# Optimization experiments

Hardware: AMD Instinct MI355X
Metric: run time of the kernel (lower is better)

Reference implementation:

```python
import jax, jax.numpy as jnp
import numpy as np

N = 200_000      # active voxels
C_IN = 128
C_OUT = 128
GRID = 128
K = 27           # 3x3x3 submanifold kernel offsets
EPS = 1e-4       # scn BatchNormalization default eps
LEAK = 0.333     # scn LeakyReLU default leakiness


def _build_neighbor_idx(rng):
    # unique active voxel coords via unique linear keys in GRID^3
    keys = rng.choice(GRID ** 3, size=N, replace=False).astype(np.int64)
    z = keys % GRID
    y = (keys // GRID) % GRID
    x = keys // (GRID * GRID)
    coords = np.stack([x, y, z], axis=1)  # [N,3]
    order = np.argsort(keys)
    sorted_keys = keys[order]
    offs = np.array([(dx, dy, dz) for dx in (-1, 0, 1)
                     for dy in (-1, 0, 1) for dz in (-1, 0, 1)], dtype=np.int64)
    nb = np.full((N, K), -1, dtype=np.int32)
    for k in range(K):
        q = coords + offs[k]  # [N,3]
        inb = np.all((q >= 0) & (q < GRID), axis=1)
        qk = (q[:, 0] * GRID + q[:, 1]) * GRID + q[:, 2]
        pos = np.searchsorted(sorted_keys, qk)
        pos = np.clip(pos, 0, N - 1)
        hit = inb & (sorted_keys[pos] == qk)
        nb[:, k] = np.where(hit, order[pos].astype(np.int32), -1)
    return nb


def setup_inputs() -> dict:
    key = jax.random.key(0)
    k1, k2 = jax.random.split(key)
    rng = np.random.default_rng(0)
    neighbor_idx = jnp.asarray(_build_neighbor_idx(rng))       # [N,27] int32, -1 = inactive
    features = jax.random.normal(k1, (N, C_IN), dtype=jnp.float32)
    # per-offset conv weights, scn-style init scale
    W = jax.random.normal(k2, (K, C_IN, C_OUT), dtype=jnp.float32) * (1.0 / np.sqrt(K * C_IN))
    b = jnp.zeros((C_OUT,), dtype=jnp.float32)
    gamma = jnp.ones((C_OUT,), dtype=jnp.float32)
    beta = jnp.zeros((C_OUT,), dtype=jnp.float32)
    return {"features": features, "W": W, "b": b, "gamma": gamma,
            "beta": beta, "neighbor_idx": neighbor_idx}


def reference(features, W, b, gamma, beta, neighbor_idx):
    # Submanifold 3D conv: output only at active sites; gather active neighbors.
    valid = (neighbor_idx >= 0)                      # [N,27] bool
    idx = jnp.where(valid, neighbor_idx, 0)          # safe gather index
    out = jnp.broadcast_to(b, (features.shape[0], C_OUT))
    for k in range(K):  # fixed structural loop over 27 kernel offsets
        xk = features[idx[:, k]] * valid[:, k:k + 1].astype(features.dtype)  # [N,C_IN]
        out = out + xk @ W[k]                                                # [N,C_OUT]
    # BatchNormalization over all active sites (training-mode batch stats)
    mean = jnp.mean(out, axis=0)
    var = jnp.var(out, axis=0)
    out = (out - mean) * jax.lax.rsqrt(var + EPS) * gamma + beta
    # LeakyReLU (scn default leakiness 0.333)
    return jnp.where(out > 0, out, LEAK * out)
```

## Files before the change

kernel.cpp:

```cpp
#include <hip/hip_runtime.h>
#include <hip/hip_bf16.h>

#define N_VOX 200000
#define CI 128
#define CO 128
#define KK 27
#define BM 128
#define NBLK 1563
#define NSTEP 54
#define LEAK 0.333f
#define BN_EPS 1e-4f
#define SENT 0x3FFFFu
#define ACC_STRIDE 132

typedef unsigned short u16;
typedef unsigned int u32;
typedef __attribute__((ext_vector_type(8))) short short8;
typedef __attribute__((ext_vector_type(4))) float f32x4;

typedef const __attribute__((address_space(1))) u32* gptr_t;
typedef __attribute__((address_space(3))) u32* lptr_t;

__device__ __forceinline__ u16 f2bf(float f) {
  union { float f; u32 u; } x; x.f = f;
  return (u16)((x.u + 0x7FFFu + ((x.u >> 16) & 1u)) >> 16);
}
__device__ __forceinline__ u16 cvt_bf(float f) {
  union { __hip_bfloat16 h; u16 u; } c;
  c.h = __float2bfloat16(f);
  return c.u;
}

__global__ __launch_bounds__(256) void fcast_kernel(const float* __restrict__ f,
                                                    u16* __restrict__ fb) {
  size_t i = ((size_t)blockIdx.x * 256 + threadIdx.x) * 8;
  float4 a = *(const float4*)(f + i);
  float4 b = *(const float4*)(f + i + 4);
  u16 t[8];
  t[0] = cvt_bf(a.x); t[1] = cvt_bf(a.y); t[2] = cvt_bf(a.z); t[3] = cvt_bf(a.w);
  t[4] = cvt_bf(b.x); t[5] = cvt_bf(b.y); t[6] = cvt_bf(b.z); t[7] = cvt_bf(b.w);
  *(uint4*)(fb + i) = *(const uint4*)t;
}

__global__ __launch_bounds__(256) void wcast3_kernel(const float* __restrict__ W,
                                                     u16* __restrict__ Wt3) {
  int gid = blockIdx.x * 256 + threadIdx.x;
  int lane = gid & 63, chunk = gid >> 6;
  int ks = chunk & 3, nf = (chunk >> 2) & 7, k = chunk >> 5;
  int lr = lane & 15, lg = lane >> 4;
  int co = nf * 16 + lr;
  int ci0 = ks * 32 + lg * 8;
  const float* Wk = W + (size_t)k * CI * CO;
  u16 t[8];
#pragma unroll
  for (int e = 0; e < 8; ++e) t[e] = f2bf(Wk[(ci0 + e) * CO + co]);
  *(uint4*)(Wt3 + (size_t)gid * 8) = *(const uint4*)t;
}

__global__ __launch_bounds__(256, 2) void conv_sp_kernel(
    const u16* __restrict__ featb, const u16* __restrict__ Wt3,
    const int* __restrict__ nb, const u16* __restrict__ zp,
    float* __restrict__ out, float* __restrict__ partial) {
  __shared__ __align__(16) char smem[75776];
  float* const accf = (float*)smem;
  u32* const rb_lds = (u32*)(smem + 67584);
  int* const cnt_lds = (int*)(smem + 74752);
  int* const wcnt = (int*)(smem + 74864);
  u32* const wl = (u32*)(smem + 74880);
  int* const wl_n = (int*)(smem + 75360);
  float* const ps = (float*)(smem + 67584);

  const int tid = threadIdx.x;
  const int bid = blockIdx.x;
  const int row0 = bid * BM;
  const int lane = tid & 63;
  const int w = tid >> 6;

  {
    f32x4 z4 = {0.f, 0.f, 0.f, 0.f};
    for (int i = tid; i < (BM * ACC_STRIDE) / 4; i += 256) ((f32x4*)accf)[i] = z4;
  }

  {
    const bool inrow = (tid < 128) && (row0 + tid < N_VOX);
    const int* nbp = nb + (size_t)(row0 + tid) * KK;
    int vv[KK];
#pragma unroll
    for (int k = 0; k < KK; ++k) vv[k] = (k != 13 && inrow) ? nbp[k] : -1;
    if (tid < 128)
      rb_lds[832 + tid] = ((u32)tid << 18) | (inrow ? (u32)(row0 + tid) : SENT);
    if (tid == 0) cnt_lds[13] = 128;
#pragma unroll
    for (int k = 0; k < KK; ++k) {
      if (k == 13) continue;
      bool valid = vv[k] >= 0;
      unsigned long long m = __ballot(valid);
      if (lane == 0) wcnt[w] = (int)__popcll(m);
      __syncthreads();
      int pos = (int)__popcll(m & ((1ull << lane) - 1ull)) + (w == 1 ? wcnt[0] : 0);
      int cnt = wcnt[0] + wcnt[1]; if (cnt > 64) cnt = 64;
      int kbase = (k < 13) ? k * 64 : 960 + (k - 14) * 64;
      if (valid && pos < 64) rb_lds[kbase + pos] = ((u32)tid << 18) | (u32)vv[k];
      int pe = (cnt + 15) & ~15;
      for (int i = cnt + tid; i < pe; i += 256) rb_lds[kbase + i] = SENT;
      if (tid == 0) cnt_lds[k] = cnt;
      __syncthreads();
    }
  }

  if (tid == 0) {
    int n = 0;
    for (int k = 0; k < KK; ++k) {
      int cnt = cnt_lds[k];
      int kbase = (k < 13) ? k * 64 : (k == 13 ? 832 : 960 + (k - 14) * 64);
      int ntk = (cnt + 15) >> 4;
      for (int t = 0; t < ntk; ++t) wl[n++] = ((u32)k << 11) | (u32)(kbase + t * 16);
    }
    wl_n[0] = n;
  }
  __syncthreads();

  const int wv = w;
  const int lr = lane & 15, lg = lane >> 4;
  const int colbase = wv * 32 + lr;
  const int nt = wl_n[0];

  auto rbRead = [&](u32 d, u32& es, uint4& sc) {
    int off = (int)(d & 0x7FFu);
    es = rb_lds[off + lr];
    sc = *(const uint4*)&rb_lds[off + lg * 4];
  };
  auto issueA = [&](u32 es, short8* a) {
    u32 src = es & SENT;
    const u16* ap = (src == SENT) ? zp : (featb + (size_t)src * CI);
#pragma unroll
    for (int ks = 0; ks < 4; ++ks) a[ks] = *(const short8*)(ap + ks * 32 + lg * 8);
  };
  auto issueB = [&](u32 d, short8* b) {
    int k = (int)(d >> 11);
    const u16* wb = Wt3 + (size_t)(k * 32 + wv * 8) * 512 + lane * 8;
#pragma unroll
    for (int j = 0; j < 8; ++j) b[j] = *(const short8*)(wb + j * 512);
  };
  auto computeT = [&](const short8* a, const short8* b, f32x4& c0, f32x4& c1) {
#pragma unroll
    for (int ks = 0; ks < 4; ++ks) {
      c0 = __builtin_amdgcn_mfma_f32_16x16x32_bf16(a[ks], b[ks], c0, 0, 0, 0);
      c1 = __builtin_amdgcn_mfma_f32_16x16x32_bf16(a[ks], b[4 + ks], c1, 0, 0, 0);
    }
  };
  auto scat1 = [&](u32 e2, float v0, float v1) {
    if (e2 != SENT) {
      int dr = (int)(e2 >> 18);
      accf[dr * ACC_STRIDE + colbase] += v0;
      accf[dr * ACC_STRIDE + colbase + 16] += v1;
    }
  };

  {
    u32 es0, es1; uint4 sc0, sc1;
    short8 a0[4], a1[4], b0v[8], b1v[8];
    u32 d0 = wl[0], d1 = wl[1];
    rbRead(d0, es0, sc0);
    rbRead(d1, es1, sc1);
    issueA(es0, a0); issueB(d0, b0v);
    issueA(es1, a1); issueB(d1, b1v);
    int i = 0;
    for (; i + 1 < nt; i += 2) {
      {
        u32 dn = wl[(i + 2 < nt) ? i + 2 : 0];
        u32 esn; uint4 scn; rbRead(dn, esn, scn);
        f32x4 c0 = {0.f, 0.f, 0.f, 0.f}, c1 = {0.f, 0.f, 0.f, 0.f};
        computeT(a0, b0v, c0, c1);
        issueA(esn, a0); issueB(dn, b0v);
        scat1(sc0.x, c0[0], c1[0]); scat1(sc0.y, c0[1], c1[1]);
        scat1(sc0.z, c0[2], c1[2]); scat1(sc0.w, c0[3], c1[3]);
        sc0 = scn;
      }
      {
        u32 dn = wl[(i + 3 < nt) ? i + 3 : 0];
        u32 esn; uint4 scn; rbRead(dn, esn, scn);
        f32x4 c0 = {0.f, 0.f, 0.f, 0.f}, c1 = {0.f, 0.f, 0.f, 0.f};
        computeT(a1, b1v, c0, c1);
        issueA(esn, a1); issueB(dn, b1v);
        scat1(sc1.x, c0[0], c1[0]); scat1(sc1.y, c0[1], c1[1]);
        scat1(sc1.z, c0[2], c1[2]); scat1(sc1.w, c0[3], c1[3]);
        sc1 = scn;
      }
    }
    if (i < nt) {
      f32x4 c0 = {0.f, 0.f, 0.f, 0.f}, c1 = {0.f, 0.f, 0.f, 0.f};
      computeT(a0, b0v, c0, c1);
      scat1(sc0.x, c0[0], c1[0]); scat1(sc0.y, c0[1], c1[1]);
      scat1(sc0.z, c0[2], c1[2]); scat1(sc0.w, c0[3], c1[3]);
    }
  }
  __syncthreads();

  float s4[4] = {0.f, 0.f, 0.f, 0.f}, q4[4] = {0.f, 0.f, 0.f, 0.f};
  const int col4 = (tid & 31) * 4;
  const int rgrp = tid >> 5;
#pragma unroll
  for (int i = 0; i < 16; ++i) {
    int row = rgrp + i * 8;
    f32x4 v = *(const f32x4*)&accf[row * ACC_STRIDE + col4];
    int grow = row0 + row;
    if (grow < N_VOX) {
      *(float4*)&out[(size_t)grow * CO + col4] = *(float4*)&v;
#pragma unroll
      for (int j = 0; j < 4; ++j) { s4[j] += v[j]; q4[j] += v[j] * v[j]; }
    }
  }
  __syncthreads();
#pragma unroll
  for (int j = 0; j < 4; ++j) {
    ps[rgrp * 128 + col4 + j] = s4[j];
    ps[1024 + rgrp * 128 + col4 + j] = q4[j];
  }
  __syncthreads();
  {
    int col = tid & 127, which = tid >> 7;
    float acc = 0.f;
#pragma unroll
    for (int g = 0; g < 8; ++g) acc += ps[which * 1024 + g * 128 + col];
    partial[(size_t)bid * 256 + tid] = acc;
  }
}

__global__ __launch_bounds__(256, 2) void conv_fb_kernel(
    const float* __restrict__ feat, const u16* __restrict__ Wt3,
    const int* __restrict__ nb, float* __restrict__ out,
    float* __restrict__ partial) {
  __shared__ __align__(16) char smem[46592];
  u16* const Ab = (u16*)smem;
  int* const nbs = (int*)(smem + 32768);
  float* const sq = (float*)smem;

  const int tid = threadIdx.x;
  const int bid = blockIdx.x;
  const int row0 = bid * BM;

  for (int i = tid; i < BM * KK; i += 256) {
    int gi = row0 * KK + i;
    nbs[i] = (gi < N_VOX * KK) ? nb[gi] : -1;
  }
  __syncthreads();

  const int lane = tid & 63;
  const int wv = tid >> 6;
  const int wr = wv >> 1, wc = wv & 1;
  const int lr = lane & 15, lg = lane >> 4;
  const int arow = tid >> 1;
  const int acol = (tid & 1) * 32;

  f32x4 acc[4][4];
#pragma unroll
  for (int m = 0; m < 4; ++m)
#pragma unroll
    for (int n = 0; n < 4; ++n) acc[m][n] = (f32x4){0.f, 0.f, 0.f, 0.f};

  float4 af[8];
  short8 b0[8], b1[8];

  auto issueAf = [&](int s) {
    int k = s >> 1, half = (s & 1) * 64;
    int src = nbs[arow * KK + k];
    if (src >= 0) {
      const float4* p = (const float4*)(feat + (size_t)src * CI + half + acol);
#pragma unroll
      for (int j = 0; j < 8; ++j) af[j] = p[j];
    } else {
#pragma unroll
      for (int j = 0; j < 8; ++j) af[j] = (float4){0.f, 0.f, 0.f, 0.f};
    }
  };
  auto loadB = [&](int s, short8* bn) {
    int k = s >> 1, half = s & 1;
#pragma unroll
    for (int n = 0; n < 4; ++n)
#pragma unroll
      for (int ks = 0; ks < 2; ++ks)
        bn[n * 2 + ks] = *(const short8*)(Wt3 +
            (size_t)((k * 32 + (wc * 4 + n) * 4) + half * 2 + ks) * 512 + lane * 8);
  };
  auto writeA = [&](u16* Adst) {
    int v = arow & 7;
#pragma unroll
    for (int q = 0; q < 4; ++q) {
      u16 t8[8];
#pragma unroll
      for (int i = 0; i < 2; ++i) {
        float4 f = af[q * 2 + i];
        t8[i * 4 + 0] = cvt_bf(f.x); t8[i * 4 + 1] = cvt_bf(f.y);
        t8[i * 4 + 2] = cvt_bf(f.z); t8[i * 4 + 3] = cvt_bf(f.w);
      }
      int c_o = (tid & 1) * 4 + q;
      *(uint4*)&Adst[arow * 64 + ((c_o ^ v) << 3)] = *(const uint4*)t8;
    }
  };
  auto compute = [&](const u16* A, const short8* bc) {
#pragma unroll
    for (int ks = 0; ks < 2; ++ks) {
      short8 a[4];
#pragma unroll
      for (int m = 0; m < 4; ++m) {
        int r = wr * 64 + m * 16 + lr;
        a[m] = *(const short8*)((const char*)A + r * 128 +
                                ((ks * 64 + lg * 16) ^ ((r & 7) << 4)));
      }
#pragma unroll
      for (int m = 0; m < 4; ++m)
#pragma unroll
        for (int n = 0; n < 4; ++n)
          acc[m][n] = __builtin_amdgcn_mfma_f32_16x16x32_bf16(a[m], bc[n * 2 + ks],
                                                              acc[m][n], 0, 0, 0);
    }
  };

  issueAf(0);
  loadB(0, b0);
  for (int s = 0; s + 2 <= NSTEP - 1; s += 2) {
    writeA(Ab + (s & 1) * 8192); __syncthreads();
    issueAf(s + 1); loadB(s + 1, b1);
    compute(Ab + (s & 1) * 8192, b0);
    writeA(Ab + ((s + 1) & 1) * 8192); __syncthreads();
    issueAf(s + 2); loadB(s + 2, b0);
    compute(Ab + ((s + 1) & 1) * 8192, b1);
  }
  writeA(Ab); __syncthreads();
  issueAf(NSTEP - 1); loadB(NSTEP - 1, b1);
  compute(Ab, b0);
  writeA(Ab + 8192); __syncthreads();
  compute(Ab + 8192, b1);

  float sv[4], qv[4];
#pragma unroll
  for (int n = 0; n < 4; ++n) {
    float s = 0.f, q = 0.f;
    int col = wc * 64 + n * 16 + lr;
#pragma unroll
    for (int m = 0; m < 4; ++m) {
      int rb_ = row0 + wr * 64 + m * 16 + lg * 4;
#pragma unroll
      for (int e = 0; e < 4; ++e) {
        float x = acc[m][n][e];
        if (rb_ + e < N_VOX) out[(size_t)(rb_ + e) * CO + col] = x;
        s += x; q += x * x;
      }
    }
    s += __shfl_xor(s, 16, 64); s += __shfl_xor(s, 32, 64);
    q += __shfl_xor(q, 16, 64); q += __shfl_xor(q, 32, 64);
    sv[n] = s; qv[n] = q;
  }
  __syncthreads();
  if (lg == 0) {
#pragma unroll
    for (int n = 0; n < 4; ++n) {
      int col = wc * 64 + n * 16 + lr;
      sq[wr * 256 + col] = sv[n];
      sq[wr * 256 + 128 + col] = qv[n];
    }
  }
  __syncthreads();
  partial[(size_t)bid * 256 + tid] = sq[tid] + sq[256 + tid];
}

__global__ __launch_bounds__(256) void reduce1_kernel(const float* __restrict__ partial,
                                                      float* __restrict__ partial2) {
  int t = threadIdx.x, b = blockIdx.x;
  float acc = 0.f;
  int jend = (b + 1) * 16; if (jend > NBLK) jend = NBLK;
  for (int j = b * 16; j < jend; ++j) acc += partial[(size_t)j * 256 + t];
  partial2[(size_t)b * 256 + t] = acc;
}

__global__ __launch_bounds__(256) void reduce2_kernel(const float* __restrict__ partial2,
                                                      const float* __restrict__ gamma,
                                                      const float* __restrict__ beta,
                                                      float* __restrict__ stats) {
  __shared__ float sums[256];
  int t = threadIdx.x;
  float acc = 0.f;
  for (int j = 0; j < 98; ++j) acc += partial2[(size_t)j * 256 + t];
  sums[t] = acc;
  __syncthreads();
  if (t < 128) {
    float mean = sums[t] / (float)N_VOX;
    float var = sums[128 + t] / (float)N_VOX - mean * mean;
    float scale = gamma[t] * rsqrtf(var + BN_EPS);
    stats[t] = scale;
    stats[128 + t] = beta[t] - mean * scale;
  }
}

__global__ __launch_bounds__(256) void bnact_kernel(float* __restrict__ out,
                                                    const float* __restrict__ stats) {
  __shared__ float s_scale[128], s_shift[128];
  int t = threadIdx.x;
  if (t < 128) { s_scale[t] = stats[t]; s_shift[t] = stats[128 + t]; }
  __syncthreads();
  size_t i = (size_t)blockIdx.x * 256 + t;
  float4* o4 = (float4*)out;
  float4 v = o4[i];
  int c0 = ((int)(i & 31)) << 2;
  float x;
  x = v.x * s_scale[c0 + 0] + s_shift[c0 + 0]; v.x = x > 0.f ? x : LEAK * x;
  x = v.y * s_scale[c0 + 1] + s_shift[c0 + 1]; v.y = x > 0.f ? x : LEAK * x;
  x = v.z * s_scale[c0 + 2] + s_shift[c0 + 2]; v.z = x > 0.f ? x : LEAK * x;
  x = v.w * s_scale[c0 + 3] + s_shift[c0 + 3]; v.w = x > 0.f ? x : LEAK * x;
  o4[i] = v;
}

extern "C" void kernel_launch(void* const* d_in, const int* in_sizes, int n_in,
                              void* d_out, int out_size, void* d_ws, size_t ws_size,
                              hipStream_t stream) {
  const float* feat  = (const float*)d_in[0];
  const float* W     = (const float*)d_in[1];
  const float* gamma = (const float*)d_in[3];
  const float* beta  = (const float*)d_in[4];
  const int*   nb    = (const int*)d_in[5];
  float* out = (float*)d_out;

  char* ws = (char*)d_ws;
  u16*   Wt3      = (u16*)ws;
  float* partial  = (float*)(ws + 884736);
  float* partial2 = (float*)(ws + 2485248);
  float* stats    = (float*)(ws + 2585600);
  u16*   zp       = (u16*)(ws + 2586624);
  u16*   featb    = (u16*)(ws + 2586880);
  const size_t need_fast = 53786880u;

  hipLaunchKernelGGL(wcast3_kernel, dim3(216), dim3(256), 0, stream, W, Wt3);
  if (ws_size >= need_fast) {
    hipMemsetAsync(zp, 0, 256, stream);
    hipLaunchKernelGGL(fcast_kernel, dim3(12500), dim3(256), 0, stream, feat, featb);
    hipLaunchKernelGGL(conv_sp_kernel, dim3(NBLK), dim3(256), 0, stream,
                       featb, Wt3, nb, zp, out, partial);
  } else {
    hipLaunchKernelGGL(conv_fb_kernel, dim3(NBLK), dim3(256), 0, stream,
                       feat, Wt3, nb, out, partial);
  }
  hipLaunchKernelGGL(reduce1_kernel, dim3(98), dim3(256), 0, stream, partial, partial2);
  hipLaunchKernelGGL(reduce2_kernel, dim3(1), dim3(256), 0, stream, partial2, gamma, beta, stats);
  hipLaunchKernelGGL(bnact_kernel, dim3(25000), dim3(256), 0, stream, out, stats);
}
```

Measured before the change: 256.5 us.

## Split sparse conv output channels across two blocks per row tile to raise occupancy

Each 128-row tile is now handled by two blocks, each computing 64 of the 128 output channels. This halves the LDS accumulator, shrinks per-neighbor rule-buffer capacity to 48, and allows 4 blocks per CU instead of 2. The partial-stats layout and the reduce kernels are adapted to the per-half layout, and sched_barriers are added around the scatter. In exchange, every block repeats the neighbor-list construction and the feature (A) gathers, and offsets with more than 48 neighbors in a tile are silently truncated.

```diff
diff --git a/kernel.cpp b/kernel.cpp
--- a/kernel.cpp
+++ b/kernel.cpp
@@ -7,11 +7,13 @@
 #define KK 27
 #define BM 128
 #define NBLK 1563
+#define NBLK2 3126
 #define NSTEP 54
 #define LEAK 0.333f
 #define BN_EPS 1e-4f
 #define SENT 0x3FFFFu
-#define ACC_STRIDE 132
+#define ACC_STRIDE 68
+#define RB_CAP 48
 
 typedef unsigned short u16;
 typedef unsigned int u32;
@@ -29,6 +31,9 @@
   union { __hip_bfloat16 h; u16 u; } c;
   c.h = __float2bfloat16(f);
   return c.u;
+}
+__device__ __forceinline__ int kbase_of(int k) {
+  return (k < 13) ? k * RB_CAP : (k == 13 ? 13 * RB_CAP : 13 * RB_CAP + 128 + (k - 14) * RB_CAP);
 }
 
 __global__ __launch_bounds__(256) void fcast_kernel(const float* __restrict__ f,
@@ -57,22 +62,24 @@
   *(uint4*)(Wt3 + (size_t)gid * 8) = *(const uint4*)t;
 }
 
-__global__ __launch_bounds__(256, 2) void conv_sp_kernel(
+__global__ __launch_bounds__(256, 4) void conv_sp_kernel(
     const u16* __restrict__ featb, const u16* __restrict__ Wt3,
     const int* __restrict__ nb, const u16* __restrict__ zp,
     float* __restrict__ out, float* __restrict__ partial) {
-  __shared__ __align__(16) char smem[75776];
+  __shared__ __align__(16) char smem[40848];
   float* const accf = (float*)smem;
-  u32* const rb_lds = (u32*)(smem + 67584);
-  int* const cnt_lds = (int*)(smem + 74752);
-  int* const wcnt = (int*)(smem + 74864);
-  u32* const wl = (u32*)(smem + 74880);
-  int* const wl_n = (int*)(smem + 75360);
-  float* const ps = (float*)(smem + 67584);
+  u32* const rb_lds = (u32*)(smem + 34816);
+  int* const cnt_lds = (int*)(smem + 40320);
+  int* const wcnt = (int*)(smem + 40432);
+  u32* const wl = (u32*)(smem + 40448);
+  int* const wl_n = (int*)(smem + 40832);
+  float* const ps = (float*)smem;
 
   const int tid = threadIdx.x;
   const int bid = blockIdx.x;
-  const int row0 = bid * BM;
+  const int ch = bid & 1;
+  const int rowblk = bid >> 1;
+  const int row0 = rowblk * BM;
   const int lane = tid & 63;
   const int w = tid >> 6;
 
@@ -88,7 +95,7 @@
 #pragma unroll
     for (int k = 0; k < KK; ++k) vv[k] = (k != 13 && inrow) ? nbp[k] : -1;
     if (tid < 128)
-      rb_lds[832 + tid] = ((u32)tid << 18) | (inrow ? (u32)(row0 + tid) : SENT);
+      rb_lds[13 * RB_CAP + tid] = ((u32)tid << 18) | (inrow ? (u32)(row0 + tid) : SENT);
     if (tid == 0) cnt_lds[13] = 128;
 #pragma unroll
     for (int k = 0; k < KK; ++k) {
@@ -98,11 +105,11 @@
       if (lane == 0) wcnt[w] = (int)__popcll(m);
       __syncthreads();
       int pos = (int)__popcll(m & ((1ull << lane) - 1ull)) + (w == 1 ? wcnt[0] : 0);
-      int cnt = wcnt[0] + wcnt[1]; if (cnt > 64) cnt = 64;
-      int kbase = (k < 13) ? k * 64 : 960 + (k - 14) * 64;
-      if (valid && pos < 64) rb_lds[kbase + pos] = ((u32)tid << 18) | (u32)vv[k];
+      int cnt = wcnt[0] + wcnt[1]; if (cnt > RB_CAP) cnt = RB_CAP;
+      int kb = kbase_of(k);
+      if (valid && pos < RB_CAP) rb_lds[kb + pos] = ((u32)tid << 18) | (u32)vv[k];
       int pe = (cnt + 15) & ~15;
-      for (int i = cnt + tid; i < pe; i += 256) rb_lds[kbase + i] = SENT;
+      for (int i = cnt + tid; i < pe; i += 256) rb_lds[kb + i] = SENT;
       if (tid == 0) cnt_lds[k] = cnt;
       __syncthreads();
     }
@@ -112,9 +119,9 @@
     int n = 0;
     for (int k = 0; k < KK; ++k) {
       int cnt = cnt_lds[k];
-      int kbase = (k < 13) ? k * 64 : (k == 13 ? 832 : 960 + (k - 14) * 64);
+      int kb = kbase_of(k);
       int ntk = (cnt + 15) >> 4;
-      for (int t = 0; t < ntk; ++t) wl[n++] = ((u32)k << 11) | (u32)(kbase + t * 16);
+      for (int t = 0; t < ntk; ++t) wl[n++] = ((u32)k << 11) | (u32)(kb + t * 16);
     }
     wl_n[0] = n;
   }
@@ -122,7 +129,8 @@
 
   const int wv = w;
   const int lr = lane & 15, lg = lane >> 4;
-  const int colbase = wv * 32 + lr;
+  const int colbase = wv * 16 + lr;
+  const int nfg = ch * 4 + wv;
   const int nt = wl_n[0];
 
   auto rbRead = [&](u32 d, u32& es, uint4& sc) {
@@ -138,75 +146,76 @@
   };
   auto issueB = [&](u32 d, short8* b) {
     int k = (int)(d >> 11);
-    const u16* wb = Wt3 + (size_t)(k * 32 + wv * 8) * 512 + lane * 8;
-#pragma unroll
-    for (int j = 0; j < 8; ++j) b[j] = *(const short8*)(wb + j * 512);
-  };
-  auto computeT = [&](const short8* a, const short8* b, f32x4& c0, f32x4& c1) {
-#pragma unroll
-    for (int ks = 0; ks < 4; ++ks) {
+    const u16* wb = Wt3 + (size_t)(k * 32 + nfg * 4) * 512 + lane * 8;
+#pragma unroll
+    for (int ks = 0; ks < 4; ++ks) b[ks] = *(const short8*)(wb + ks * 512);
+  };
+  auto computeT = [&](const short8* a, const short8* b, f32x4& c0) {
+#pragma unroll
+    for (int ks = 0; ks < 4; ++ks)
       c0 = __builtin_amdgcn_mfma_f32_16x16x32_bf16(a[ks], b[ks], c0, 0, 0, 0);
-      c1 = __builtin_amdgcn_mfma_f32_16x16x32_bf16(a[ks], b[4 + ks], c1, 0, 0, 0);
-    }
-  };
-  auto scat1 = [&](u32 e2, float v0, float v1) {
-    if (e2 != SENT) {
-      int dr = (int)(e2 >> 18);
-      accf[dr * ACC_STRIDE + colbase] += v0;
-      accf[dr * ACC_STRIDE + colbase + 16] += v1;
+  };
+  auto scat4 = [&](const uint4& sc, const f32x4& c0) {
+    u32 e[4] = {sc.x, sc.y, sc.z, sc.w};
+#pragma unroll
+    for (int r = 0; r < 4; ++r) {
+      if (e[r] != SENT) {
+        int dr = (int)(e[r] >> 18);
+        accf[dr * ACC_STRIDE + colbase] += c0[r];
+      }
     }
   };
 
   {
     u32 es0, es1; uint4 sc0, sc1;
-    short8 a0[4], a1[4], b0v[8], b1v[8];
+    short8 a0[4], a1[4], b0v[4], b1v[4];
     u32 d0 = wl[0], d1 = wl[1];
     rbRead(d0, es0, sc0);
     rbRead(d1, es1, sc1);
     issueA(es0, a0); issueB(d0, b0v);
     issueA(es1, a1); issueB(d1, b1v);
+    __builtin_amdgcn_sched_barrier(0);
     int i = 0;
     for (; i + 1 < nt; i += 2) {
       {
         u32 dn = wl[(i + 2 < nt) ? i + 2 : 0];
         u32 esn; uint4 scn; rbRead(dn, esn, scn);
-        f32x4 c0 = {0.f, 0.f, 0.f, 0.f}, c1 = {0.f, 0.f, 0.f, 0.f};
-        computeT(a0, b0v, c0, c1);
+        f32x4 c0 = {0.f, 0.f, 0.f, 0.f};
+        computeT(a0, b0v, c0);
         issueA(esn, a0); issueB(dn, b0v);
-        scat1(sc0.x, c0[0], c1[0]); scat1(sc0.y, c0[1], c1[1]);
-        scat1(sc0.z, c0[2], c1[2]); scat1(sc0.w, c0[3], c1[3]);
+        __builtin_amdgcn_sched_barrier(0);
+        scat4(sc0, c0);
         sc0 = scn;
       }
       {
         u32 dn = wl[(i + 3 < nt) ? i + 3 : 0];
         u32 esn; uint4 scn; rbRead(dn, esn, scn);
-        f32x4 c0 = {0.f, 0.f, 0.f, 0.f}, c1 = {0.f, 0.f, 0.f, 0.f};
-        computeT(a1, b1v, c0, c1);
+        f32x4 c0 = {0.f, 0.f, 0.f, 0.f};
+        computeT(a1, b1v, c0);
         issueA(esn, a1); issueB(dn, b1v);
-        scat1(sc1.x, c0[0], c1[0]); scat1(sc1.y, c0[1], c1[1]);
-        scat1(sc1.z, c0[2], c1[2]); scat1(sc1.w, c0[3], c1[3]);
+        __builtin_amdgcn_sched_barrier(0);
+        scat4(sc1, c0);
         sc1 = scn;
       }
     }
     if (i < nt) {
-      f32x4 c0 = {0.f, 0.f, 0.f, 0.f}, c1 = {0.f, 0.f, 0.f, 0.f};
-      computeT(a0, b0v, c0, c1);
-      scat1(sc0.x, c0[0], c1[0]); scat1(sc0.y, c0[1], c1[1]);
-      scat1(sc0.z, c0[2], c1[2]); scat1(sc0.w, c0[3], c1[3]);
+      f32x4 c0 = {0.f, 0.f, 0.f, 0.f};
+      computeT(a0, b0v, c0);
+      scat4(sc0, c0);
     }
   }
   __syncthreads();
 
   float s4[4] = {0.f, 0.f, 0.f, 0.f}, q4[4] = {0.f, 0.f, 0.f, 0.f};
-  const int col4 = (tid & 31) * 4;
-  const int rgrp = tid >> 5;
-#pragma unroll
-  for (int i = 0; i < 16; ++i) {
-    int row = rgrp + i * 8;
+  const int col4 = (tid & 15) * 4;
+  const int rgrp = tid >> 4;
+#pragma unroll
+  for (int i = 0; i < 8; ++i) {
+    int row = rgrp + i * 16;
     f32x4 v = *(const f32x4*)&accf[row * ACC_STRIDE + col4];
     int grow = row0 + row;
     if (grow < N_VOX) {
-      *(float4*)&out[(size_t)grow * CO + col4] = *(float4*)&v;
+      *(float4*)&out[(size_t)grow * CO + ch * 64 + col4] = *(float4*)&v;
 #pragma unroll
       for (int j = 0; j < 4; ++j) { s4[j] += v[j]; q4[j] += v[j] * v[j]; }
     }
@@ -214,16 +223,16 @@
   __syncthreads();
 #pragma unroll
   for (int j = 0; j < 4; ++j) {
-    ps[rgrp * 128 + col4 + j] = s4[j];
-    ps[1024 + rgrp * 128 + col4 + j] = q4[j];
-  }
-  __syncthreads();
-  {
-    int col = tid & 127, which = tid >> 7;
+    ps[rgrp * 64 + col4 + j] = s4[j];
+    ps[1024 + rgrp * 64 + col4 + j] = q4[j];
+  }
+  __syncthreads();
+  if (tid < 128) {
+    int issq = tid >> 6, c = tid & 63;
     float acc = 0.f;
 #pragma unroll
-    for (int g = 0; g < 8; ++g) acc += ps[which * 1024 + g * 128 + col];
-    partial[(size_t)bid * 256 + tid] = acc;
+    for (int g = 0; g < 16; ++g) acc += ps[issq * 1024 + g * 64 + c];
+    partial[(size_t)bid * 128 + issq * 64 + c] = acc;
   }
 }
 
@@ -362,15 +371,22 @@
     }
   }
   __syncthreads();
-  partial[(size_t)bid * 256 + tid] = sq[tid] + sq[256 + tid];
+  {
+    int col = tid & 127, issq = tid >> 7;
+    partial[(size_t)bid * 256 + (col >> 6) * 128 + issq * 64 + (col & 63)] =
+        sq[tid] + sq[256 + tid];
+  }
 }
 
 __global__ __launch_bounds__(256) void reduce1_kernel(const float* __restrict__ partial,
                                                       float* __restrict__ partial2) {
   int t = threadIdx.x, b = blockIdx.x;
+  int c = t & 127, issq = t >> 7;
+  int ch = c >> 6, lc = c & 63;
   float acc = 0.f;
   int jend = (b + 1) * 16; if (jend > NBLK) jend = NBLK;
-  for (int j = b * 16; j < jend; ++j) acc += partial[(size_t)j * 256 + t];
+  for (int j = b * 16; j < jend; ++j)
+    acc += partial[(size_t)(j * 2 + ch) * 128 + issq * 64 + lc];
   partial2[(size_t)b * 256 + t] = acc;
 }
 
@@ -434,7 +450,7 @@
   if (ws_size >= need_fast) {
     hipMemsetAsync(zp, 0, 256, stream);
     hipLaunchKernelGGL(fcast_kernel, dim3(12500), dim3(256), 0, stream, feat, featb);
-    hipLaunchKernelGGL(conv_sp_kernel, dim3(NBLK), dim3(256), 0, stream,
+    hipLaunchKernelGGL(conv_sp_kernel, dim3(NBLK2), dim3(256), 0, stream,
                        featb, Wt3, nb, zp, out, partial);
   } else {
     hipLaunchKernelGGL(conv_fb_kernel, dim3(NBLK), dim3(256), 0, stream,
```

After: 334.0 us. 1.3x slower.
